# Kernel optimization log

Hardware: AMD Instinct MI355X
Metric: run time of the kernel (lower is better)

The kernel has to match this reference:

```python
import jax, jax.numpy as jnp
import numpy as np


def _hfreq_mask(c, scale):
    # zeros over the centered (shifted) low-frequency band, ones elsewhere
    m = np.ones((c,), dtype=np.complex64)
    m[c // 2 - c // scale: c // 2 + c // scale] = 0
    return jnp.asarray(m).reshape(1, 1, 1, c)


def setup_inputs() -> dict:
    key = jax.random.key(0)
    x = jax.random.normal(key, (32, 38, 38, 728), dtype=jnp.float32)
    return {"x": x, "scale": 4}


def reference(x, scale):
    c = x.shape[-1]
    norm = jnp.asarray(np.sqrt(c), dtype=jnp.complex64)
    X = jnp.fft.fft(x.astype(jnp.complex64), axis=-1) / norm
    X = jnp.fft.fftshift(X, axes=-1)
    X = X * _hfreq_mask(c, scale)
    X = jnp.fft.ifftshift(X, axes=-1)
    y = jnp.fft.ifft(X, axis=-1) * norm
    y = jnp.real(y).astype(jnp.float32)
    return jax.nn.relu(y)
```

## Files before the change

### kernel.cpp

```cpp
#include <hip/hip_runtime.h>
#include <hip/hip_bf16.h>

#define CC 728
#define PP 364
#define KP 384
#define M_ROWS 46208
#define KT 12
#define NWG 2166

typedef __attribute__((ext_vector_type(8))) short bf16x8;
typedef __attribute__((ext_vector_type(8))) unsigned short ushort8;
typedef __attribute__((ext_vector_type(4))) float f32x4;

__device__ __forceinline__ unsigned short f2bf(float f) {
    unsigned int u = __float_as_uint(f);
    unsigned int r = u + 0x7fffu + ((u >> 16) & 1u);
    return (unsigned short)(r >> 16);
}

__device__ __forceinline__ void gload_lds16(const void* g, void* l) {
    __builtin_amdgcn_global_load_lds(
        (const __attribute__((address_space(1))) void*)g,
        (__attribute__((address_space(3))) void*)l,
        16, 0, 0);
}

__global__ void build_bt(unsigned short* __restrict__ bt1,
                         unsigned short* __restrict__ bt2) {
    int idx = blockIdx.x * blockDim.x + threadIdx.x;
    if (idx >= 2 * KP * KP) return;
    int mat = idx / (KP * KP);
    int rem = idx % (KP * KP);
    int n = rem / KP, k = rem % KP;
    float v = 0.f;
    if (n < PP && k < PP) {
        int m = n - k - (mat == 0 ? 1 : 0);
        if (m < 0) m += PP;
        int d = 2 * m + 1;
        float t = (float)(3.14159265358979323846 * (double)d / (double)CC);
        float s = ((d >> 1) & 1) ? 1.f : -1.f;
        v = s * cosf(t) / ((float)CC * sinf(t));
    }
    (mat == 0 ? bt1 : bt2)[n * KP + k] = f2bf(v);
}

__global__ __launch_bounds__(256) void gemm_relu(
        const float* __restrict__ x,
        const unsigned short* __restrict__ bt1,
        const unsigned short* __restrict__ bt2,
        float* __restrict__ out) {
    __shared__ unsigned short ldsE[3][64 * 32];
    __shared__ unsigned short ldsO[3][64 * 32];
    __shared__ unsigned short ldsB1[3][128 * 32];
    __shared__ unsigned short ldsB2[3][128 * 32];

    const int tid  = threadIdx.x;
    const int lane = tid & 63;
    const int wid  = tid >> 6;
    const int wr   = wid >> 1, wc = wid & 1;
    const int l15  = lane & 15, lhi = lane >> 4;

    const int NX = 8;
    int orig = blockIdx.x;
    int q = NWG / NX, r = NWG % NX;
    int xcd = orig % NX, local = orig / NX;
    int wgid = (xcd < r ? xcd * (q + 1) : r * (q + 1) + (xcd - r) * q) + local;
    const int bm  = (wgid / 3) * 64;
    const int bnp = (wgid % 3) * 128;

    f32x4 acc_e[2][4], acc_o[2][4];
#pragma unroll
    for (int i = 0; i < 2; ++i)
#pragma unroll
        for (int j = 0; j < 4; ++j)
#pragma unroll
            for (int rr = 0; rr < 4; ++rr) { acc_e[i][j][rr] = 0.f; acc_o[i][j][rr] = 0.f; }

    const int brow = tid >> 2;
    const int bc   = tid & 3;
    const int arow = tid >> 2;
    const int acx  = tid & 3;

    auto stageB = [&](int buf, int kt) {
        int k0 = kt * 32;
#pragma unroll
        for (int i = 0; i < 2; ++i) {
            int rr   = i * 64 + brow;
            int gsrc = (bc - (rr >> 1)) & 3;
            size_t so = (size_t)(bnp + rr) * KP + k0 + gsrc * 8;
            gload_lds16(bt1 + so, &ldsB1[buf][(i * 256 + tid) * 8]);
            gload_lds16(bt2 + so, &ldsB2[buf][(i * 256 + tid) * 8]);
        }
    };
    auto loadA = [&](int kt, float4* va) {
        int cb0 = kt * 64 + acx * 16;
        const float* src = x + (size_t)(bm + arow) * CC + cb0;
#pragma unroll
        for (int i = 0; i < 4; ++i)
            va[i] = (cb0 + 4 * i < CC) ? ((const float4*)src)[i]
                                       : make_float4(0.f, 0.f, 0.f, 0.f);
    };
    auto writeA = [&](int buf, const float4* va) {
        ushort8 oe, oo;
#pragma unroll
        for (int p = 0; p < 4; ++p) {
            float4 f = va[p];
            oe[2 * p]     = f2bf(f.x); oo[2 * p]     = f2bf(f.y);
            oe[2 * p + 1] = f2bf(f.z); oo[2 * p + 1] = f2bf(f.w);
        }
        int sc = (acx + (arow >> 1)) & 3;
        *(ushort8*)&ldsE[buf][arow * 32 + sc * 8] = oe;
        *(ushort8*)&ldsO[buf][arow * 32 + sc * 8] = oo;
    };

    float4 va[2][4];
    loadA(0, va[0]); stageB(0, 0);
    loadA(1, va[1]); stageB(1, 1);

#pragma unroll
    for (int kt = 0; kt < KT; ++kt) {
        const int cur = kt % 3;
        const int nx2 = (kt + 2) % 3;

        asm volatile("s_waitcnt vmcnt(8)" ::: "memory");
        writeA(cur, va[kt & 1]);
        asm volatile("s_waitcnt lgkmcnt(0)" ::: "memory");
        __builtin_amdgcn_s_barrier();
        __builtin_amdgcn_sched_barrier(0);

        const int kpre = (kt + 2 < KT) ? (kt + 2) : 10;
        loadA(kpre, va[kt & 1]);
        stageB(nx2, kpre);

        bf16x8 aE[2], aO[2], b1[4], b2[4];
#pragma unroll
        for (int mi = 0; mi < 2; ++mi) {
            int row = wr * 32 + mi * 16 + l15;
            int c   = (lhi + (row >> 1)) & 3;
            aE[mi] = *(const bf16x8*)&ldsE[cur][row * 32 + c * 8];
            aO[mi] = *(const bf16x8*)&ldsO[cur][row * 32 + c * 8];
        }
#pragma unroll
        for (int nj = 0; nj < 4; ++nj) {
            int row = wc * 64 + nj * 16 + l15;
            int c   = (lhi + (row >> 1)) & 3;
            b1[nj] = *(const bf16x8*)&ldsB1[cur][row * 32 + c * 8];
            b2[nj] = *(const bf16x8*)&ldsB2[cur][row * 32 + c * 8];
        }
        __builtin_amdgcn_s_setprio(1);
#pragma unroll
        for (int mi = 0; mi < 2; ++mi)
#pragma unroll
            for (int nj = 0; nj < 4; ++nj) {
                acc_e[mi][nj] = __builtin_amdgcn_mfma_f32_16x16x32_bf16(
                    aO[mi], b1[nj], acc_e[mi][nj], 0, 0, 0);
                acc_o[mi][nj] = __builtin_amdgcn_mfma_f32_16x16x32_bf16(
                    aE[mi], b2[nj], acc_o[mi][nj], 0, 0, 0);
            }
        __builtin_amdgcn_s_setprio(0);
    }

#pragma unroll
    for (int mi = 0; mi < 2; ++mi) {
#pragma unroll
        for (int nj = 0; nj < 4; ++nj) {
            int colp = bnp + wc * 64 + nj * 16 + l15;
            if (colp < PP) {
#pragma unroll
                for (int rr = 0; rr < 4; ++rr) {
                    int rowg = bm + wr * 32 + mi * 16 + lhi * 4 + rr;
                    size_t base = (size_t)rowg * CC + 2 * colp;
                    float2 xv = *(const float2*)&x[base];
                    float2 o;
                    float ye = 0.5f * xv.x + acc_e[mi][nj][rr];
                    float yo = 0.5f * xv.y + acc_o[mi][nj][rr];
                    o.x = ye > 0.f ? ye : 0.f;
                    o.y = yo > 0.f ? yo : 0.f;
                    *(float2*)&out[base] = o;
                }
            }
        }
    }
}

extern "C" void kernel_launch(void* const* d_in, const int* in_sizes, int n_in,
                              void* d_out, int out_size, void* d_ws, size_t ws_size,
                              hipStream_t stream) {
    const float* x = (const float*)d_in[0];
    float* out = (float*)d_out;

    unsigned short* bt1 = (unsigned short*)d_ws;
    unsigned short* bt2 = bt1 + KP * KP;

    build_bt<<<(2 * KP * KP + 255) / 256, 256, 0, stream>>>(bt1, bt2);
    gemm_relu<<<NWG, 256, 0, stream>>>(x, bt1, bt2, out);
}
```

Before: 107.8 us.

## Restructure GEMM pipeline to single A buffer and double-buffered B

Replaces the triple-buffered LDS pipeline with a prefetch-depth-two schedule: a single LDS slot for the converted A tile and two slots for the B tiles, with two barriers per k-step. The smaller LDS footprint is meant to let more workgroups fit per CU and so raise occupancy. In exchange the pipeline gets shallower and gains an extra barrier per iteration, which can expose global memory latency. The f2bf return type change is cosmetic.

```diff
diff --git a/kernel.cpp b/kernel.cpp
--- a/kernel.cpp
+++ b/kernel.cpp
@@ -4,18 +4,18 @@
 #define CC 728
 #define PP 364
 #define KP 384
+#define KT 12
 #define M_ROWS 46208
-#define KT 12
 #define NWG 2166
 
 typedef __attribute__((ext_vector_type(8))) short bf16x8;
 typedef __attribute__((ext_vector_type(8))) unsigned short ushort8;
 typedef __attribute__((ext_vector_type(4))) float f32x4;
 
-__device__ __forceinline__ unsigned short f2bf(float f) {
+__device__ __forceinline__ unsigned int f2bf(float f) {
     unsigned int u = __float_as_uint(f);
     unsigned int r = u + 0x7fffu + ((u >> 16) & 1u);
-    return (unsigned short)(r >> 16);
+    return r >> 16;
 }
 
 __device__ __forceinline__ void gload_lds16(const void* g, void* l) {
@@ -41,7 +41,7 @@
         float s = ((d >> 1) & 1) ? 1.f : -1.f;
         v = s * cosf(t) / ((float)CC * sinf(t));
     }
-    (mat == 0 ? bt1 : bt2)[n * KP + k] = f2bf(v);
+    (mat == 0 ? bt1 : bt2)[n * KP + k] = (unsigned short)f2bf(v);
 }
 
 __global__ __launch_bounds__(256) void gemm_relu(
@@ -49,10 +49,10 @@
         const unsigned short* __restrict__ bt1,
         const unsigned short* __restrict__ bt2,
         float* __restrict__ out) {
-    __shared__ unsigned short ldsE[3][64 * 32];
-    __shared__ unsigned short ldsO[3][64 * 32];
-    __shared__ unsigned short ldsB1[3][128 * 32];
-    __shared__ unsigned short ldsB2[3][128 * 32];
+    __shared__ unsigned short ldsE[64 * 32];
+    __shared__ unsigned short ldsO[64 * 32];
+    __shared__ unsigned short ldsB1[2][128 * 32];
+    __shared__ unsigned short ldsB2[2][128 * 32];
 
     const int tid  = threadIdx.x;
     const int lane = tid & 63;
@@ -92,7 +92,7 @@
             gload_lds16(bt2 + so, &ldsB2[buf][(i * 256 + tid) * 8]);
         }
     };
-    auto loadA = [&](int kt, float4* va) {
+    auto loadA = [&](int kt, float4 (&va)[4]) {
         int cb0 = kt * 64 + acx * 16;
         const float* src = x + (size_t)(bm + arow) * CC + cb0;
 #pragma unroll
@@ -100,52 +100,35 @@
             va[i] = (cb0 + 4 * i < CC) ? ((const float4*)src)[i]
                                        : make_float4(0.f, 0.f, 0.f, 0.f);
     };
-    auto writeA = [&](int buf, const float4* va) {
+    auto writeA = [&](const float4 (&va)[4]) {
         ushort8 oe, oo;
 #pragma unroll
         for (int p = 0; p < 4; ++p) {
             float4 f = va[p];
-            oe[2 * p]     = f2bf(f.x); oo[2 * p]     = f2bf(f.y);
-            oe[2 * p + 1] = f2bf(f.z); oo[2 * p + 1] = f2bf(f.w);
+            oe[2 * p]     = (unsigned short)f2bf(f.x);
+            oo[2 * p]     = (unsigned short)f2bf(f.y);
+            oe[2 * p + 1] = (unsigned short)f2bf(f.z);
+            oo[2 * p + 1] = (unsigned short)f2bf(f.w);
         }
         int sc = (acx + (arow >> 1)) & 3;
-        *(ushort8*)&ldsE[buf][arow * 32 + sc * 8] = oe;
-        *(ushort8*)&ldsO[buf][arow * 32 + sc * 8] = oo;
-    };
-
-    float4 va[2][4];
-    loadA(0, va[0]); stageB(0, 0);
-    loadA(1, va[1]); stageB(1, 1);
-
-#pragma unroll
-    for (int kt = 0; kt < KT; ++kt) {
-        const int cur = kt % 3;
-        const int nx2 = (kt + 2) % 3;
-
-        asm volatile("s_waitcnt vmcnt(8)" ::: "memory");
-        writeA(cur, va[kt & 1]);
-        asm volatile("s_waitcnt lgkmcnt(0)" ::: "memory");
-        __builtin_amdgcn_s_barrier();
-        __builtin_amdgcn_sched_barrier(0);
-
-        const int kpre = (kt + 2 < KT) ? (kt + 2) : 10;
-        loadA(kpre, va[kt & 1]);
-        stageB(nx2, kpre);
-
+        *(ushort8*)&ldsE[arow * 32 + sc * 8] = oe;
+        *(ushort8*)&ldsO[arow * 32 + sc * 8] = oo;
+    };
+    auto compute = [&](int buf) {
         bf16x8 aE[2], aO[2], b1[4], b2[4];
 #pragma unroll
         for (int mi = 0; mi < 2; ++mi) {
             int row = wr * 32 + mi * 16 + l15;
             int c   = (lhi + (row >> 1)) & 3;
-            aE[mi] = *(const bf16x8*)&ldsE[cur][row * 32 + c * 8];
-            aO[mi] = *(const bf16x8*)&ldsO[cur][row * 32 + c * 8];
+            aE[mi] = *(const bf16x8*)&ldsE[row * 32 + c * 8];
+            aO[mi] = *(const bf16x8*)&ldsO[row * 32 + c * 8];
         }
 #pragma unroll
         for (int nj = 0; nj < 4; ++nj) {
             int row = wc * 64 + nj * 16 + l15;
             int c   = (lhi + (row >> 1)) & 3;
-            b1[nj] = *(const bf16x8*)&ldsB1[cur][row * 32 + c * 8];
-            b2[nj] = *(const bf16x8*)&ldsB2[cur][row * 32 + c * 8];
+            b1[nj] = *(const bf16x8*)&ldsB1[buf][row * 32 + c * 8];
+            b2[nj] = *(const bf16x8*)&ldsB2[buf][row * 32 + c * 8];
         }
         __builtin_amdgcn_s_setprio(1);
 #pragma unroll
@@ -158,6 +141,35 @@
                     aE[mi], b2[nj], acc_o[mi][nj], 0, 0, 0);
             }
         __builtin_amdgcn_s_setprio(0);
+    };
+
+    auto step = [&](int t, const float4 (&vaCur)[4], float4 (&vaNxt)[4],
+                    int curbuf, int nxtbuf) {
+        asm volatile("s_waitcnt vmcnt(4)" ::: "memory");
+        __builtin_amdgcn_s_barrier();
+        __builtin_amdgcn_sched_barrier(0);
+        writeA(vaCur);
+        if (t + 1 < KT) {
+            loadA(t + 1, vaNxt);
+            stageB(nxtbuf, t + 1);
+            asm volatile("s_waitcnt vmcnt(8)" ::: "memory");
+        } else {
+            asm volatile("s_waitcnt vmcnt(0)" ::: "memory");
+        }
+        asm volatile("s_waitcnt lgkmcnt(0)" ::: "memory");
+        __builtin_amdgcn_s_barrier();
+        __builtin_amdgcn_sched_barrier(0);
+        compute(curbuf);
+    };
+
+    float4 vaA[4], vaB[4];
+    loadA(0, vaA);
+    stageB(0, 0);
+
+#pragma unroll
+    for (int tp = 0; tp < KT / 2; ++tp) {
+        step(2 * tp,     vaA, vaB, 0, 1);
+        step(2 * tp + 1, vaB, vaA, 1, 0);
     }
 
 #pragma unroll
```

New measurement: 107.1 us. Within noise of the previous version (-0.6%).
